# Optimization experiments

Measured on AMD Instinct MI355X. Metric: run time of the kernel, lower is better.

Reference implementation:

```python
import jax, jax.numpy as jnp
import numpy as np

EPS = 1e-5
NUM_HEADS = 16


def _rmsnorm(x, w, eps=EPS):
    var = jnp.mean(jnp.square(x), axis=-1, keepdims=True)
    return x * jax.lax.rsqrt(var + eps) * w


def setup_inputs() -> dict:
    key = jax.random.key(0)
    ks = jax.random.split(key, 7)
    B, T, H = 4, 8192, 1024
    KD, VD = 512, 1024          # key_dim = 0.5*H, value_dim = H
    hk, hv = KD // NUM_HEADS, VD // NUM_HEADS  # 32, 64
    return {
        "hidden_states": jax.random.normal(ks[0], (B, T, H), jnp.float32),
        "recurrent_state": jax.random.normal(ks[1], (B, NUM_HEADS, hk, hv), jnp.float32),
        "norm_w": jax.random.uniform(ks[2], (H,), jnp.float32, 0.5, 1.5),
        "q_w": jax.random.normal(ks[3], (KD, H), jnp.float32) * 0.02,
        "v_norm_w": jax.random.uniform(ks[4], (hv,), jnp.float32, 0.5, 1.5),
        "o_w": jax.random.normal(ks[5], (H, VD), jnp.float32) * 0.02,
        "gate_w": jax.random.normal(ks[6], (H, H), jnp.float32) * 0.02,
    }


def reference(hidden_states, recurrent_state, norm_w, q_w, v_norm_w, o_w, gate_w):
    B, T, H = hidden_states.shape
    nh = NUM_HEADS
    x = _rmsnorm(hidden_states, norm_w)                      # [B,T,H]
    q = (x @ q_w.T).reshape(B, T, nh, -1)                    # [B,T,h,dk]
    # F.normalize(dim=-1): divide by max(L2 norm, 1e-12)
    q = q / jnp.maximum(jnp.linalg.norm(q, axis=-1, keepdims=True), 1e-12)
    o = jnp.einsum('bthk,bhkv->bthv', q, recurrent_state)    # [B,T,h,dv]
    o = _rmsnorm(o, v_norm_w)
    o = o.reshape(B, T, -1) @ o_w.T                          # [B,T,H]
    gate = jax.nn.sigmoid(x @ gate_w.T)                      # [B,T,H]
    return gate * o
```

## Files before the change

kernel.cpp:

```cpp
#include <hip/hip_runtime.h>
#include <hip/hip_bf16.h>
#include <stdint.h>

typedef __attribute__((ext_vector_type(8))) short short8;
typedef __attribute__((ext_vector_type(4))) float floatx4;
typedef __attribute__((ext_vector_type(2))) unsigned int uint2v;

#define DEV static __device__ __forceinline__

DEV unsigned short f2bs(float f) {
  union { float f; unsigned u; } v; v.f = f;
  unsigned u = v.u;
  u += 0x7fffu + ((u >> 16) & 1u);
  return (unsigned short)(u >> 16);
}
DEV float bs2f(unsigned short s) {
  union { unsigned u; float f; } v; v.u = ((unsigned)s) << 16;
  return v.f;
}
DEV unsigned pack2(float a, float b) {
  return (unsigned)f2bs(a) | ((unsigned)f2bs(b) << 16);
}

DEV void gload_lds16(const void* g, void* l) {
  __builtin_amdgcn_global_load_lds(
      (const __attribute__((address_space(1))) void*)g,
      (__attribute__((address_space(3))) void*)l, 16, 0, 0);
}

static constexpr int Hdim = 1024;
static constexpr int KDim = 512;
static constexpr int NH = 16;
static constexpr int HK = 32;
static constexpr int HV = 64;
static constexpr int Mtok = 4 * 8192;

__global__ __launch_bounds__(256) void k_cvt(const float4* __restrict__ in,
                                             uint2v* __restrict__ out, int n4) {
  int i = blockIdx.x * 256 + threadIdx.x;
  if (i >= n4) return;
  float4 v = in[i];
  uint2v o;
  o.x = pack2(v.x, v.y);
  o.y = pack2(v.z, v.w);
  out[i] = o;
}

__global__ __launch_bounds__(256) void k_cvts(const float* __restrict__ S,
                                              unsigned short* __restrict__ St) {
  int i = blockIdx.x * 256 + threadIdx.x;
  if (i >= 4 * NH * HV * HK) return;
  int k = i & 31, v = (i >> 5) & 63, bh = i >> 11;
  St[i] = f2bs(S[(size_t)(bh * HK + k) * HV + v]);
}

__global__ __launch_bounds__(256) void k_rmsnorm(const float* __restrict__ hs,
                                                 const float* __restrict__ nw,
                                                 uint2v* __restrict__ X) {
  const int token = blockIdx.x;
  const int tid = threadIdx.x;
  float4 h = ((const float4*)(hs + (size_t)token * Hdim))[tid];
  float ss = h.x * h.x + h.y * h.y + h.z * h.z + h.w * h.w;
#pragma unroll
  for (int off = 32; off > 0; off >>= 1) ss += __shfl_down(ss, off, 64);
  __shared__ float red[4];
  const int lane = tid & 63, wid = tid >> 6;
  if (lane == 0) red[wid] = ss;
  __syncthreads();
  float tot = red[0] + red[1] + red[2] + red[3];
  float sc = rsqrtf(tot * (1.0f / Hdim) + 1e-5f);
  float4 w = ((const float4*)nw)[tid];
  uint2v o;
  o.x = pack2(h.x * sc * w.x, h.y * sc * w.y);
  o.y = pack2(h.z * sc * w.z, h.w * sc * w.w);
  X[(size_t)token * 256 + tid] = o;
}

DEV void gemm128s(const unsigned short* __restrict__ A,
                  const unsigned short* __restrict__ Bw, const int K,
                  const int m0, const int n0, unsigned short* As,
                  unsigned short* Bs, floatx4 (&acc)[4][4], const int tid) {
  const int lane = tid & 63;
  const int w = tid >> 6;
  const int wr = w >> 1, wc = w & 1;
  const int frr = lane & 15;
  const int frk = (lane >> 4) * 8;
  const int aswz = (frr & 7) * 8;
  const int r_a = tid >> 3;
  const int c_src = ((tid & 7) ^ (r_a & 7)) * 8;
  const unsigned short* Ag = A + (size_t)(m0 + r_a) * K + c_src;
  const unsigned short* Bg = Bw + (size_t)(n0 + r_a) * K + c_src;
  char* AsDst = (char*)As + tid * 16;
  char* BsDst = (char*)Bs + tid * 16;

  for (int k0 = 0; k0 < K; k0 += 64) {
#pragma unroll
    for (int i = 0; i < 4; ++i)
      gload_lds16(Ag + (size_t)i * 32 * K + k0, AsDst + i * 4096);
#pragma unroll
    for (int i = 0; i < 4; ++i)
      gload_lds16(Bg + (size_t)i * 32 * K + k0, BsDst + i * 4096);
    __syncthreads();
#pragma unroll
    for (int kk = 0; kk < 2; ++kk) {
      short8 a[4], b[4];
#pragma unroll
      for (int mi = 0; mi < 4; ++mi)
        a[mi] = *(const short8*)
            &As[(wr * 64 + mi * 16 + frr) * 64 + ((kk * 32 + frk) ^ aswz)];
#pragma unroll
      for (int ni = 0; ni < 4; ++ni)
        b[ni] = *(const short8*)
            &Bs[(wc * 64 + ni * 16 + frr) * 64 + ((kk * 32 + frk) ^ aswz)];
#pragma unroll
      for (int mi = 0; mi < 4; ++mi)
#pragma unroll
        for (int ni = 0; ni < 4; ++ni)
          acc[mi][ni] = __builtin_amdgcn_mfma_f32_16x16x32_bf16(
              a[mi], b[ni], acc[mi][ni], 0, 0, 0);
    }
    __syncthreads();
  }
}

__global__ __launch_bounds__(256, 3) void k_fused_go(
    const unsigned short* __restrict__ X, const unsigned short* __restrict__ Ob,
    const unsigned short* __restrict__ gwb,
    const unsigned short* __restrict__ owb, float* __restrict__ out) {
  __shared__ unsigned short As[128 * 64];
  __shared__ unsigned short Bs[128 * 64];
  const int tid = threadIdx.x;
  const int lane = tid & 63;
  const int w = tid >> 6;
  const int wr = w >> 1, wc = w & 1;
  const int bid = blockIdx.x;
  const int v = (bid & 7) * 256 + (bid >> 3);
  const int m0 = (v >> 3) * 128;
  const int n0 = (v & 7) * 128;

  floatx4 acc[4][4];
#pragma unroll
  for (int i = 0; i < 4; ++i)
#pragma unroll
    for (int j = 0; j < 4; ++j) acc[i][j] = (floatx4){0.f, 0.f, 0.f, 0.f};

  gemm128s(X, gwb, Hdim, m0, n0, As, Bs, acc, tid);

  unsigned pg[4][4][2];
#pragma unroll
  for (int mi = 0; mi < 4; ++mi)
#pragma unroll
    for (int ni = 0; ni < 4; ++ni) {
      float s0 = 1.0f / (1.0f + __expf(-acc[mi][ni][0]));
      float s1 = 1.0f / (1.0f + __expf(-acc[mi][ni][1]));
      float s2 = 1.0f / (1.0f + __expf(-acc[mi][ni][2]));
      float s3 = 1.0f / (1.0f + __expf(-acc[mi][ni][3]));
      pg[mi][ni][0] = pack2(s0, s1);
      pg[mi][ni][1] = pack2(s2, s3);
      acc[mi][ni] = (floatx4){0.f, 0.f, 0.f, 0.f};
    }

  gemm128s(Ob, owb, Hdim, m0, n0, As, Bs, acc, tid);

  const int rb = (lane >> 4) * 4;
#pragma unroll
  for (int mi = 0; mi < 4; ++mi)
#pragma unroll
    for (int ni = 0; ni < 4; ++ni) {
      const int n = n0 + wc * 64 + ni * 16 + (lane & 15);
#pragma unroll
      for (int r = 0; r < 4; ++r) {
        const int m = m0 + wr * 64 + mi * 16 + rb + r;
        float g = bs2f((unsigned short)(pg[mi][ni][r >> 1] >> ((r & 1) * 16)));
        out[(size_t)m * Hdim + n] = g * acc[mi][ni][r];
      }
    }
}

__global__ __launch_bounds__(256, 3) void k_fused_q(
    const unsigned short* __restrict__ X, const unsigned short* __restrict__ qwb,
    const unsigned short* __restrict__ St, const float* __restrict__ vnw,
    unsigned short* __restrict__ Ob) {
  __shared__ unsigned short LD[128 * 128];
  unsigned short* As = LD;
  unsigned short* Bs = LD + 128 * 64;
  const int tid = threadIdx.x;
  const int lane = tid & 63;
  const int w = tid >> 6;
  const int wr = w >> 1, wc = w & 1;
  const int bid = blockIdx.x;
  const int v = (bid & 7) * 128 + (bid >> 3);
  const int m0 = (v >> 2) * 128;
  const int n0 = (v & 3) * 128;
  const int h0 = n0 >> 5;
  const int batch = m0 >> 13;

  floatx4 acc[4][4];
#pragma unroll
  for (int i = 0; i < 4; ++i)
#pragma unroll
    for (int j = 0; j < 4; ++j) acc[i][j] = (floatx4){0.f, 0.f, 0.f, 0.f};

  gemm128s(X, qwb, Hdim, m0, n0, As, Bs, acc, tid);

  const int rb = (lane >> 4) * 4;
  const int frr = lane & 15;
#pragma unroll
  for (int mi = 0; mi < 4; ++mi)
#pragma unroll
    for (int p = 0; p < 2; ++p) {
#pragma unroll
      for (int r = 0; r < 4; ++r) {
        float v0 = acc[mi][2 * p][r], v1 = acc[mi][2 * p + 1][r];
        float ss = v0 * v0 + v1 * v1;
        ss += __shfl_xor(ss, 1, 64);
        ss += __shfl_xor(ss, 2, 64);
        ss += __shfl_xor(ss, 4, 64);
        ss += __shfl_xor(ss, 8, 64);
        const float inv = 1.0f / fmaxf(sqrtf(ss), 1e-12f);
        const int m = wr * 64 + mi * 16 + rb + r;
        const int c0 = wc * 64 + p * 32 + frr;
        const int sw = (m & 7) * 8;
        LD[m * 128 + (c0 ^ sw)] = f2bs(v0 * inv);
        LD[m * 128 + ((c0 + 16) ^ sw)] = f2bs(v1 * inv);
      }
    }
  __syncthreads();

  const int frk = (lane >> 4) * 8;
  float wv[4];
#pragma unroll
  for (int ni = 0; ni < 4; ++ni) wv[ni] = vnw[ni * 16 + frr];

#pragma unroll
  for (int hh = 0; hh < 4; ++hh) {
    const unsigned short* Sp =
        St + (size_t)(batch * NH + h0 + hh) * (HV * HK);
    short8 bfr[4];
#pragma unroll
    for (int ni = 0; ni < 4; ++ni)
      bfr[ni] = *(const short8*)&Sp[(ni * 16 + frr) * HK + frk];
    floatx4 acc2[2][4];
#pragma unroll
    for (int i = 0; i < 2; ++i)
#pragma unroll
      for (int j = 0; j < 4; ++j) acc2[i][j] = (floatx4){0.f, 0.f, 0.f, 0.f};
    short8 af[2];
#pragma unroll
    for (int mi2 = 0; mi2 < 2; ++mi2) {
      const int m = w * 32 + mi2 * 16 + frr;
      af[mi2] = *(const short8*)&LD[m * 128 + ((hh * 32 + frk) ^ ((m & 7) * 8))];
    }
#pragma unroll
    for (int mi2 = 0; mi2 < 2; ++mi2)
#pragma unroll
      for (int ni = 0; ni < 4; ++ni)
        acc2[mi2][ni] = __builtin_amdgcn_mfma_f32_16x16x32_bf16(
            af[mi2], bfr[ni], acc2[mi2][ni], 0, 0, 0);

#pragma unroll
    for (int mi2 = 0; mi2 < 2; ++mi2)
#pragma unroll
      for (int r = 0; r < 4; ++r) {
        float ss2 = 0.f;
#pragma unroll
        for (int ni = 0; ni < 4; ++ni) ss2 += acc2[mi2][ni][r] * acc2[mi2][ni][r];
        ss2 += __shfl_xor(ss2, 1, 64);
        ss2 += __shfl_xor(ss2, 2, 64);
        ss2 += __shfl_xor(ss2, 4, 64);
        ss2 += __shfl_xor(ss2, 8, 64);
        const float sc = rsqrtf(ss2 * (1.0f / HV) + 1e-5f);
        const int m = m0 + w * 32 + mi2 * 16 + rb + r;
        unsigned short* Op = Ob + (size_t)m * Hdim + (h0 + hh) * HV;
#pragma unroll
        for (int ni = 0; ni < 4; ++ni)
          Op[ni * 16 + frr] = f2bs(acc2[mi2][ni][r] * sc * wv[ni]);
      }
  }
}

extern "C" void kernel_launch(void* const* d_in, const int* in_sizes, int n_in,
                              void* d_out, int out_size, void* d_ws, size_t ws_size,
                              hipStream_t stream) {
  const float* hs = (const float*)d_in[0];
  const float* Srec = (const float*)d_in[1];
  const float* nw = (const float*)d_in[2];
  const float* qw = (const float*)d_in[3];
  const float* vnw = (const float*)d_in[4];
  const float* ow = (const float*)d_in[5];
  const float* gw = (const float*)d_in[6];

  char* ws = (char*)d_ws;
  unsigned short* X = (unsigned short*)(ws);
  unsigned short* Ob = (unsigned short*)(ws + ((size_t)64 << 20));
  unsigned short* qwb = (unsigned short*)(ws + ((size_t)128 << 20));
  unsigned short* gwb = (unsigned short*)(ws + ((size_t)129 << 20));
  unsigned short* owb = (unsigned short*)(ws + ((size_t)131 << 20));
  unsigned short* Stb = (unsigned short*)(ws + ((size_t)133 << 20));

  k_cvt<<<(KDim * Hdim / 4 + 255) / 256, 256, 0, stream>>>(
      (const float4*)qw, (uint2v*)qwb, KDim * Hdim / 4);
  k_cvt<<<(Hdim * Hdim / 4 + 255) / 256, 256, 0, stream>>>(
      (const float4*)gw, (uint2v*)gwb, Hdim * Hdim / 4);
  k_cvt<<<(Hdim * Hdim / 4 + 255) / 256, 256, 0, stream>>>(
      (const float4*)ow, (uint2v*)owb, Hdim * Hdim / 4);
  k_cvts<<<(4 * NH * HV * HK + 255) / 256, 256, 0, stream>>>(Srec, Stb);

  k_rmsnorm<<<Mtok, 256, 0, stream>>>(hs, nw, (uint2v*)X);

  k_fused_q<<<(Mtok / 128) * (KDim / 128), 256, 0, stream>>>(
      X, qwb, Stb, vnw, Ob);

  k_fused_go<<<(Mtok / 128) * (Hdim / 128), 256, 0, stream>>>(
      X, Ob, gwb, owb, (float*)d_out);
}
```

Baseline: 277.6 us.

## Double-buffer LDS tiles in the shared GEMM loop to overlap loads with MFMA

Replaces the single-buffered 128x128 GEMM helper with a double-buffered version. The next K-tile is prefetched into the alternate LDS buffer while MFMAs run on the current one, with one barrier per iteration instead of two. This hides global-to-LDS load latency but doubles LDS use to 64KB per block, and launch bounds drop from 3 to 2 blocks per CU, which reduces occupancy.

```diff
diff --git a/kernel.cpp b/kernel.cpp
--- a/kernel.cpp
+++ b/kernel.cpp
@@ -76,10 +76,10 @@
   X[(size_t)token * 256 + tid] = o;
 }
 
-DEV void gemm128s(const unsigned short* __restrict__ A,
+DEV void gemm128d(const unsigned short* __restrict__ A,
                   const unsigned short* __restrict__ Bw, const int K,
-                  const int m0, const int n0, unsigned short* As,
-                  unsigned short* Bs, floatx4 (&acc)[4][4], const int tid) {
+                  const int m0, const int n0, unsigned short* LDS,
+                  floatx4 (&acc)[4][4], const int tid) {
   const int lane = tid & 63;
   const int w = tid >> 6;
   const int wr = w >> 1, wc = w & 1;
@@ -90,28 +90,46 @@
   const int c_src = ((tid & 7) ^ (r_a & 7)) * 8;
   const unsigned short* Ag = A + (size_t)(m0 + r_a) * K + c_src;
   const unsigned short* Bg = Bw + (size_t)(n0 + r_a) * K + c_src;
-  char* AsDst = (char*)As + tid * 16;
-  char* BsDst = (char*)Bs + tid * 16;
-
-  for (int k0 = 0; k0 < K; k0 += 64) {
-#pragma unroll
-    for (int i = 0; i < 4; ++i)
-      gload_lds16(Ag + (size_t)i * 32 * K + k0, AsDst + i * 4096);
-#pragma unroll
-    for (int i = 0; i < 4; ++i)
-      gload_lds16(Bg + (size_t)i * 32 * K + k0, BsDst + i * 4096);
-    __syncthreads();
+  const int NT = K >> 6;
+
+  {
+    char* AsD = (char*)LDS + tid * 16;
+    char* BsD = (char*)(LDS + 16384) + tid * 16;
+#pragma unroll
+    for (int i = 0; i < 4; ++i) {
+      gload_lds16(Ag + (size_t)i * 32 * K, AsD + i * 4096);
+      gload_lds16(Bg + (size_t)i * 32 * K, BsD + i * 4096);
+    }
+  }
+  asm volatile("s_waitcnt vmcnt(0)" ::: "memory");
+  __builtin_amdgcn_s_barrier();
+  asm volatile("" ::: "memory");
+
+  int cur = 0;
+  for (int t = 0; t < NT; ++t) {
+    if (t + 1 < NT) {
+      char* AsD = (char*)(LDS + (cur ^ 1) * 8192) + tid * 16;
+      char* BsD = (char*)(LDS + 16384 + (cur ^ 1) * 8192) + tid * 16;
+      const int k0 = (t + 1) * 64;
+#pragma unroll
+      for (int i = 0; i < 4; ++i) {
+        gload_lds16(Ag + (size_t)i * 32 * K + k0, AsD + i * 4096);
+        gload_lds16(Bg + (size_t)i * 32 * K + k0, BsD + i * 4096);
+      }
+    }
+    const unsigned short* Asb = LDS + cur * 8192;
+    const unsigned short* Bsb = LDS + 16384 + cur * 8192;
 #pragma unroll
     for (int kk = 0; kk < 2; ++kk) {
       short8 a[4], b[4];
 #pragma unroll
       for (int mi = 0; mi < 4; ++mi)
         a[mi] = *(const short8*)
-            &As[(wr * 64 + mi * 16 + frr) * 64 + ((kk * 32 + frk) ^ aswz)];
+            &Asb[(wr * 64 + mi * 16 + frr) * 64 + ((kk * 32 + frk) ^ aswz)];
 #pragma unroll
       for (int ni = 0; ni < 4; ++ni)
         b[ni] = *(const short8*)
-            &Bs[(wc * 64 + ni * 16 + frr) * 64 + ((kk * 32 + frk) ^ aswz)];
+            &Bsb[(wc * 64 + ni * 16 + frr) * 64 + ((kk * 32 + frk) ^ aswz)];
 #pragma unroll
       for (int mi = 0; mi < 4; ++mi)
 #pragma unroll
@@ -119,16 +137,21 @@
           acc[mi][ni] = __builtin_amdgcn_mfma_f32_16x16x32_bf16(
               a[mi], b[ni], acc[mi][ni], 0, 0, 0);
     }
-    __syncthreads();
+    if (t + 1 < NT) {
+      asm volatile("s_waitcnt vmcnt(0)" ::: "memory");
+      __builtin_amdgcn_s_barrier();
+      asm volatile("" ::: "memory");
+    }
+    cur ^= 1;
   }
-}
-
-__global__ __launch_bounds__(256, 3) void k_fused_go(
+  __syncthreads();
+}
+
+__global__ __launch_bounds__(256, 2) void k_fused_go(
     const unsigned short* __restrict__ X, const unsigned short* __restrict__ Ob,
     const unsigned short* __restrict__ gwb,
     const unsigned short* __restrict__ owb, float* __restrict__ out) {
-  __shared__ unsigned short As[128 * 64];
-  __shared__ unsigned short Bs[128 * 64];
+  __shared__ unsigned short LDS[4 * 128 * 64];
   const int tid = threadIdx.x;
   const int lane = tid & 63;
   const int w = tid >> 6;
@@ -144,7 +167,7 @@
 #pragma unroll
     for (int j = 0; j < 4; ++j) acc[i][j] = (floatx4){0.f, 0.f, 0.f, 0.f};
 
-  gemm128s(X, gwb, Hdim, m0, n0, As, Bs, acc, tid);
+  gemm128d(X, gwb, Hdim, m0, n0, LDS, acc, tid);
 
   unsigned pg[4][4][2];
 #pragma unroll
@@ -160,7 +183,7 @@
       acc[mi][ni] = (floatx4){0.f, 0.f, 0.f, 0.f};
     }
 
-  gemm128s(Ob, owb, Hdim, m0, n0, As, Bs, acc, tid);
+  gemm128d(Ob, owb, Hdim, m0, n0, LDS, acc, tid);
 
   const int rb = (lane >> 4) * 4;
 #pragma unroll
@@ -177,13 +200,11 @@
     }
 }
 
-__global__ __launch_bounds__(256, 3) void k_fused_q(
+__global__ __launch_bounds__(256, 2) void k_fused_q(
     const unsigned short* __restrict__ X, const unsigned short* __restrict__ qwb,
     const unsigned short* __restrict__ St, const float* __restrict__ vnw,
     unsigned short* __restrict__ Ob) {
-  __shared__ unsigned short LD[128 * 128];
-  unsigned short* As = LD;
-  unsigned short* Bs = LD + 128 * 64;
+  __shared__ unsigned short LD[4 * 128 * 64];
   const int tid = threadIdx.x;
   const int lane = tid & 63;
   const int w = tid >> 6;
@@ -201,7 +222,7 @@
 #pragma unroll
     for (int j = 0; j < 4; ++j) acc[i][j] = (floatx4){0.f, 0.f, 0.f, 0.f};
 
-  gemm128s(X, qwb, Hdim, m0, n0, As, Bs, acc, tid);
+  gemm128d(X, qwb, Hdim, m0, n0, LD, acc, tid);
 
   const int rb = (lane >> 4) * 4;
   const int frr = lane & 15;
```

Measured after the change: 262.7 us. 5.4% less time.
